# Kernel tuning notes

Measured on AMD Instinct MI355X. Metric: run time of the kernel, lower is better.

Reference implementation:

```python
import jax, jax.numpy as jnp
import numpy as np

B, CIN, H, W = 4, 1024, 64, 64
PLANES = 256
K = 3
DIL = 2
PAD = DIL * (K - 1) // 2  # = 2
EPS = 1e-5


def setup_inputs() -> dict:
    key = jax.random.key(0)
    ks = jax.random.split(key, 16)
    d = {}
    d['x'] = jax.random.normal(ks[0], (B, CIN, H, W), dtype=jnp.float32)
    # conv1: 1x1, inplanes->planes, no bias
    d['w1'] = jax.random.normal(ks[1], (PLANES, CIN), dtype=jnp.float32) * 0.02
    d['gamma1'] = jnp.ones((PLANES,), jnp.float32)
    d['beta1'] = jnp.zeros((PLANES,), jnp.float32)
    d['mean1'] = jax.random.normal(ks[2], (PLANES,), dtype=jnp.float32) * 0.1
    d['var1'] = jax.random.uniform(ks[3], (PLANES,), minval=0.5, maxval=1.5, dtype=jnp.float32)
    # deform_offset: 3x3 conv planes->18, with bias
    d['woff'] = jax.random.normal(ks[4], (18, PLANES, K, K), dtype=jnp.float32) * 0.01
    d['boff'] = jnp.zeros((18,), jnp.float32)
    # conv2 (deformable): 3x3 planes->planes, with bias
    d['w2'] = jax.random.normal(ks[5], (PLANES, PLANES, K, K), dtype=jnp.float32) * 0.02
    d['bconv2'] = jnp.zeros((PLANES,), jnp.float32)
    d['gamma2'] = jnp.ones((PLANES,), jnp.float32)
    d['beta2'] = jnp.zeros((PLANES,), jnp.float32)
    d['mean2'] = jax.random.normal(ks[6], (PLANES,), dtype=jnp.float32) * 0.1
    d['var2'] = jax.random.uniform(ks[7], (PLANES,), minval=0.5, maxval=1.5, dtype=jnp.float32)
    # conv3: 1x1 planes->planes*4, no bias
    d['w3'] = jax.random.normal(ks[8], (PLANES * 4, PLANES), dtype=jnp.float32) * 0.02
    d['gamma3'] = jnp.ones((PLANES * 4,), jnp.float32)
    d['beta3'] = jnp.zeros((PLANES * 4,), jnp.float32)
    d['mean3'] = jax.random.normal(ks[9], (PLANES * 4,), dtype=jnp.float32) * 0.1
    d['var3'] = jax.random.uniform(ks[10], (PLANES * 4,), minval=0.5, maxval=1.5, dtype=jnp.float32)
    return d


def _bn(x, gamma, beta, mean, var):
    # inference-mode BatchNorm over channel dim (NCHW)
    inv = jax.lax.rsqrt(var + EPS)
    return (x - mean[:, None, None]) * (inv * gamma)[:, None, None] + beta[:, None, None]


def _deform_conv(x, offset, w, b):
    # x: [B,C,H,W]; offset: [B,18,H,W] ordered (dy,dx) per kernel tap; w: [O,C,3,3]
    Bn, C, Hh, Ww = x.shape
    off = offset.reshape(Bn, K * K, 2, Hh, Ww)
    off_y, off_x = off[:, :, 0], off[:, :, 1]          # [B,9,H,W]
    kk = jnp.arange(K * K)
    base_y = (kk // K) * DIL - PAD                      # [9]
    base_x = (kk % K) * DIL - PAD
    ys = jnp.arange(Hh, dtype=x.dtype)
    xs = jnp.arange(Ww, dtype=x.dtype)
    py = base_y.astype(x.dtype)[None, :, None, None] + ys[None, None, :, None] + off_y
    px = base_x.astype(x.dtype)[None, :, None, None] + xs[None, None, None, :] + off_x

    def sample_one(img, py1, px1):
        # img [C,H,W]; py1/px1 [9,H,W] -> [C,9,H,W] bilinear with zero padding
        y0 = jnp.floor(py1)
        x0 = jnp.floor(px1)
        wy = py1 - y0
        wx = px1 - x0

        def gather(yc, xc):
            yi = yc.astype(jnp.int32)
            xi = xc.astype(jnp.int32)
            valid = ((yi >= 0) & (yi < Hh) & (xi >= 0) & (xi < Ww)).astype(img.dtype)
            yi = jnp.clip(yi, 0, Hh - 1)
            xi = jnp.clip(xi, 0, Ww - 1)
            return img[:, yi, xi] * valid[None]

        v00 = gather(y0, x0)
        v01 = gather(y0, x0 + 1)
        v10 = gather(y0 + 1, x0)
        v11 = gather(y0 + 1, x0 + 1)
        return (v00 * ((1 - wy) * (1 - wx))[None] + v01 * ((1 - wy) * wx)[None]
                + v10 * (wy * (1 - wx))[None] + v11 * (wy * wx)[None])

    sampled = jax.vmap(sample_one)(x, py, px)           # [B,C,9,H,W]
    out = jnp.einsum('bckhw,ock->bohw', sampled, w.reshape(w.shape[0], C, K * K))
    return out + b[None, :, None, None]


def reference(x, w1, gamma1, beta1, mean1, var1, woff, boff, w2, bconv2,
              gamma2, beta2, mean2, var2, w3, gamma3, beta3, mean3, var3):
    residual = x
    out = jnp.einsum('bchw,oc->bohw', x, w1)            # conv1 1x1
    out = jax.nn.relu(_bn(out, gamma1, beta1, mean1, var1))
    offset = jax.lax.conv_general_dilated(
        out, woff, window_strides=(1, 1), padding=((PAD, PAD), (PAD, PAD)),
        rhs_dilation=(DIL, DIL), dimension_numbers=('NCHW', 'OIHW', 'NCHW'))
    offset = offset + boff[None, :, None, None]
    out = _deform_conv(out, offset, w2, bconv2)
    out = jax.nn.relu(_bn(out, gamma2, beta2, mean2, var2))
    out = jnp.einsum('bchw,oc->bohw', out, w3)          # conv3 1x1
    out = _bn(out, gamma3, beta3, mean3, var3)
    return jax.nn.relu(out + residual)
```

## Files before the change

kernel.cpp:

```cpp
#include <hip/hip_runtime.h>

#define EPS_BN 1e-5f

typedef __bf16 bf16x8 __attribute__((ext_vector_type(8)));
typedef float f32x4 __attribute__((ext_vector_type(4)));

__device__ __forceinline__ unsigned short f2bf(float f) {
  union { float f; unsigned u; } v; v.f = f;
  unsigned r = v.u + 0x7fffu + ((v.u >> 16) & 1u);
  return (unsigned short)(r >> 16);
}
__device__ __forceinline__ float bf2f(unsigned short h) {
  union { unsigned u; float f; } v; v.u = ((unsigned)h) << 16;
  return v.f;
}

__global__ __launch_bounds__(256) void prep_all(
    const float* __restrict__ w1, const float* __restrict__ w2, const float* __restrict__ woff,
    const float* __restrict__ w3,
    const float* g1, const float* b1, const float* m1, const float* v1,
    const float* g2, const float* b2, const float* m2, const float* v2, const float* bconv2,
    const float* g3, const float* b3, const float* m3, const float* v3,
    unsigned short* __restrict__ w1b, unsigned short* __restrict__ w2r,
    uint4* __restrict__ act1Pz, unsigned short* __restrict__ wob,
    unsigned short* __restrict__ w3b, float* __restrict__ shift3,
    float* s1, float* h1, float* s2, float* h2) {
  int bid = blockIdx.x, tid = threadIdx.x;
  if (bid < 1024) {
    int i = bid * 256 + tid;
    w1b[i] = f2bf(w1[i]);
  } else if (bid < 3328) {
    int i = (bid - 1024) * 256 + tid;
    int o = i / 2304, r = i % 2304;
    int kk = r / 256, c = r % 256;
    w2r[i] = f2bf(w2[(size_t)o * 2304 + c * 9 + kk]);
  } else if (bid < 3592) {
    int i = (bid - 3328) * 256 + tid;
    int cell = i >> 5, q = i & 31;
    int b = cell / 528, r = cell - b * 528;
    int row, col;
    if (r < 136) { row = r / 68; col = r % 68; }
    else if (r < 272) { int rr = r - 136; row = 66 + rr / 68; col = rr % 68; }
    else { int rr = r - 272; row = 2 + (rr >> 2); int c4 = rr & 3; col = (c4 < 2) ? c4 : c4 + 64; }
    act1Pz[(((size_t)(b * 68) + row) * 68 + col) * 32 + q] = uint4{0, 0, 0, 0};
  } else if (bid < 3880) {
    int i = (bid - 3592) * 256 + tid;
    int o = i / 2304, r = i % 2304;
    int kk = r / 256, c = r % 256;
    wob[i] = (o < 18) ? f2bf(woff[(size_t)o * 2304 + c * 9 + kk]) : (unsigned short)0;
  } else if (bid < 4904) {
    int i = (bid - 3880) * 256 + tid;
    int o = i >> 8;
    float sc = rsqrtf(v3[o] + EPS_BN) * g3[o];
    w3b[i] = f2bf(w3[i] * sc);
  } else if (bid < 4908) {
    int c = (bid - 4904) * 256 + tid;
    float sc = rsqrtf(v3[c] + EPS_BN) * g3[c];
    shift3[c] = b3[c] - m3[c] * sc;
  } else {
    int c = tid;
    float sc1 = rsqrtf(v1[c] + EPS_BN) * g1[c];
    s1[c] = sc1; h1[c] = b1[c] - m1[c] * sc1;
    float sc2 = rsqrtf(v2[c] + EPS_BN) * g2[c];
    s2[c] = sc2; h2[c] = b2[c] + (bconv2[c] - m2[c]) * sc2;
  }
}

__global__ __launch_bounds__(256) void gemm1_x(
    const float* __restrict__ x, const unsigned short* __restrict__ Bm,
    unsigned short* __restrict__ part, int KH) {
  __shared__ __align__(16) char blob[16896];
  __shared__ __align__(16) unsigned short sA1[4096];
  __shared__ __align__(16) unsigned short sB1[4096];
  unsigned short* sA0 = (unsigned short*)blob;
  unsigned short* sB0 = (unsigned short*)(blob + 8192);
  float* tbuf = (float*)blob;
  int tid = threadIdx.x, lane = tid & 63, wv = tid >> 6;
  int z = blockIdx.z;
  int m0 = blockIdx.y * 128, n0 = blockIdx.x * 128;
  f32x4 acc[4][4] = {};
  int rowB = tid >> 2;
  int kcolBs = (((tid & 3) ^ (rowB & 3))) * 8;
  int px = tid & 127, chalf = tid >> 7;
  int s0w = (chalf * 2) ^ (px & 3), s1w = (chalf * 2 + 1) ^ (px & 3);
  int bb = m0 >> 12, p0 = m0 & 4095;
  const float* xa = x + (size_t)bb * 4194304 + (size_t)(chalf * 16) * 4096 + (p0 + px);
  int wm = wv & 1, wn = wv >> 1;
  int lane15 = lane & 15, quad = lane >> 4, l3 = lane & 3;

  float va[16];

#define G1_ISSUE_A(K0)                                                                    \
  {                                                                                       \
    const float* xp = xa + (size_t)(K0) * 4096;                                           \
    _Pragma("unroll") for (int j = 0; j < 16; ++j) va[j] = xp[(size_t)j * 4096];          \
  }

#define G1_ISSUE_B(DB, K0)                                                                \
  {                                                                                       \
    _Pragma("unroll") for (int r = 0; r < 2; ++r) {                                       \
      const unsigned short* gp = Bm + (size_t)(n0 + r * 64 + rowB) * 1024 + (K0) + kcolBs;\
      __builtin_amdgcn_global_load_lds((const __attribute__((address_space(1))) void*)gp, \
          (__attribute__((address_space(3))) void*)&(DB)[r * 2048 + wv * 512], 16, 0, 0); \
    }                                                                                     \
  }

#define G1_CVT_WRITE(DA)                                                                  \
  {                                                                                       \
    unsigned o8[8];                                                                       \
    _Pragma("unroll") for (int j = 0; j < 8; ++j)                                         \
      o8[j] = (unsigned)f2bf(va[2 * j]) | ((unsigned)f2bf(va[2 * j + 1]) << 16);          \
    *(uint4*)((DA) + px * 32 + s0w * 8) = uint4{o8[0], o8[1], o8[2], o8[3]};              \
    *(uint4*)((DA) + px * 32 + s1w * 8) = uint4{o8[4], o8[5], o8[6], o8[7]};              \
  }

#define G1_COMPUTE(DA, DB)                                                                \
  {                                                                                       \
    bf16x8 afr[4], bfr[4];                                                                \
    _Pragma("unroll") for (int mi = 0; mi < 4; ++mi)                                      \
      afr[mi] = *(const bf16x8*)&(DA)[(wm * 64 + mi * 16 + lane15) * 32 + (quad ^ l3) * 8]; \
    _Pragma("unroll") for (int ni = 0; ni < 4; ++ni)                                      \
      bfr[ni] = *(const bf16x8*)&(DB)[(wn * 64 + ni * 16 + lane15) * 32 + (quad ^ l3) * 8]; \
    _Pragma("unroll") for (int mi = 0; mi < 4; ++mi)                                      \
      _Pragma("unroll") for (int ni = 0; ni < 4; ++ni)                                    \
        acc[mi][ni] =                                                                     \
            __builtin_amdgcn_mfma_f32_16x16x32_bf16(afr[mi], bfr[ni], acc[mi][ni], 0, 0, 0); \
  }

#define G1_BODY(K0, AC, BC, AN, BN_)                                                      \
  {                                                                                       \
    G1_ISSUE_A(K0);                                                                       \
    G1_ISSUE_B(BN_, K0);                                                                  \
    asm volatile("s_waitcnt vmcnt(18)" ::: "memory");                                     \
    asm volatile("s_waitcnt lgkmcnt(0)" ::: "memory");                                    \
    __builtin_amdgcn_s_barrier();                                                         \
    G1_COMPUTE(AC, BC);                                                                   \
    asm volatile("s_waitcnt vmcnt(2)" ::: "memory");                                      \
    G1_CVT_WRITE(AN);                                                                     \
    __builtin_amdgcn_s_barrier();                                                         \
  }

  int kbase = z * KH;
  int nst = KH >> 5;
  G1_ISSUE_A(kbase);
  G1_ISSUE_B(sB0, kbase);
  asm volatile("s_waitcnt vmcnt(2)" ::: "memory");
  G1_CVT_WRITE(sA0);
  for (int t = 0; t + 2 < nst; t += 2) {
    G1_BODY(kbase + (t + 1) * 32, sA0, sB0, sA1, sB1);
    G1_BODY(kbase + (t + 2) * 32, sA1, sB1, sA0, sB0);
  }
  G1_BODY(kbase + (nst - 1) * 32, sA0, sB0, sA1, sB1);
  asm volatile("s_waitcnt vmcnt(0)" ::: "memory");
  asm volatile("s_waitcnt lgkmcnt(0)" ::: "memory");
  __builtin_amdgcn_s_barrier();
  G1_COMPUTE(sA1, sB1);
#undef G1_ISSUE_A
#undef G1_ISSUE_B
#undef G1_CVT_WRITE
#undef G1_COMPUTE
#undef G1_BODY

  unsigned short* outH = part + (size_t)z * 16384 * 256;
  int trow = tid >> 3;
  int tcol16 = (tid & 7) * 16;
  int growBase = m0 + (trow >> 4) * 64 + (trow & 15);
#pragma unroll
  for (int mi = 0; mi < 4; ++mi) {
    __syncthreads();
#pragma unroll
    for (int ni = 0; ni < 4; ++ni)
#pragma unroll
      for (int reg = 0; reg < 4; ++reg)
        tbuf[(wm * 16 + quad * 4 + reg) * 132 + wn * 64 + ni * 16 + lane15] = acc[mi][ni][reg];
    __syncthreads();
    int gr = growBase + mi * 16;
    const float* lp = &tbuf[trow * 132 + tcol16];
    unsigned o[8];
#pragma unroll
    for (int j = 0; j < 8; ++j)
      o[j] = (unsigned)f2bf(lp[2 * j]) | ((unsigned)f2bf(lp[2 * j + 1]) << 16);
    unsigned short* op = outH + (size_t)gr * 256 + n0 + tcol16;
    *(uint4*)(op) = uint4{o[0], o[1], o[2], o[3]};
    *(uint4*)(op + 8) = uint4{o[4], o[5], o[6], o[7]};
  }
}

__global__ __launch_bounds__(256) void gemm_split(
    const unsigned short* __restrict__ A, const unsigned short* __restrict__ Bm,
    unsigned short* __restrict__ part, int M, int N, int K, int KH) {
  __shared__ __align__(16) char blob[16896];
  __shared__ __align__(16) unsigned short sA1[4096];
  __shared__ __align__(16) unsigned short sB1[4096];
  __shared__ __align__(16) unsigned short sA2[4096];
  __shared__ __align__(16) unsigned short sB2[4096];
  __shared__ __align__(16) unsigned short sA3[4096];
  __shared__ __align__(16) unsigned short sB3[4096];
  unsigned short* sA0 = (unsigned short*)blob;
  unsigned short* sB0 = (unsigned short*)(blob + 8192);
  float* tbuf = (float*)blob;
  int tid = threadIdx.x, lane = tid & 63, wv = tid >> 6;
  int z = blockIdx.z;
  int m0 = blockIdx.y * 128, n0 = blockIdx.x * 128;
  f32x4 acc[4][4] = {};
  int rowA = tid >> 2;
  int kcolS = (((tid & 3) ^ (rowA & 3))) * 8;
  int wm = wv & 1, wn = wv >> 1;
  int lane15 = lane & 15, quad = lane >> 4, l3 = lane & 3;

#define GS_STAGE(dA, dB, K0)                                                              \
  {                                                                                       \
    int k0_ = (K0);                                                                       \
    _Pragma("unroll") for (int r = 0; r < 2; ++r) {                                       \
      const unsigned short* gp = A + (size_t)(m0 + r * 64 + rowA) * K + k0_ + kcolS;      \
      __builtin_amdgcn_global_load_lds((const __attribute__((address_space(1))) void*)gp, \
          (__attribute__((address_space(3))) void*)&(dA)[r * 2048 + wv * 512], 16, 0, 0); \
    }                                                                                     \
    _Pragma("unroll") for (int r = 0; r < 2; ++r) {                                       \
      const unsigned short* gp = Bm + (size_t)(n0 + r * 64 + rowA) * K + k0_ + kcolS;     \
      __builtin_amdgcn_global_load_lds((const __attribute__((address_space(1))) void*)gp, \
          (__attribute__((address_space(3))) void*)&(dB)[r * 2048 + wv * 512], 16, 0, 0); \
    }                                                                                     \
  }

#define GS_COMPUTE(dA, dB)                                                                \
  {                                                                                       \
    bf16x8 afr[4], bfr[4];                                                                \
    _Pragma("unroll") for (int mi = 0; mi < 4; ++mi)                                      \
      afr[mi] = *(const bf16x8*)&(dA)[(wm * 64 + mi * 16 + lane15) * 32 + (quad ^ l3) * 8]; \
    _Pragma("unroll") for (int ni = 0; ni < 4; ++ni)                                      \
      bfr[ni] = *(const bf16x8*)&(dB)[(wn * 64 + ni * 16 + lane15) * 32 + (quad ^ l3) * 8]; \
    _Pragma("unroll") for (int mi = 0; mi < 4; ++mi)                                      \
      _Pragma("unroll") for (int ni = 0; ni < 4; ++ni)                                    \
        acc[mi][ni] =                                                                     \
            __builtin_amdgcn_mfma_f32_16x16x32_bf16(afr[mi], bfr[ni], acc[mi][ni], 0, 0, 0); \
  }

#define GS_STEP8(AC, BC, SN, AN, BN_)                                                     \
  {                                                                                       \
    GS_STAGE(AN, BN_, kbase + (SN) * 32);                                                 \
    asm volatile("s_waitcnt vmcnt(8)" ::: "memory");                                      \
    __builtin_amdgcn_s_barrier();                                                         \
    GS_COMPUTE(AC, BC);                                                                   \
    __builtin_amdgcn_s_barrier();                                                         \
  }

  int kbase = z * KH;
  int nst = KH >> 5;
  GS_STAGE(sA0, sB0, kbase);
  GS_STAGE(sA1, sB1, kbase + 32);
  for (int s4 = 0; s4 < nst - 4; s4 += 4) {
    GS_STEP8(sA0, sB0, s4 + 2, sA2, sB2);
    GS_STEP8(sA1, sB1, s4 + 3, sA3, sB3);
    GS_STEP8(sA2, sB2, s4 + 4, sA0, sB0);
    GS_STEP8(sA3, sB3, s4 + 5, sA1, sB1);
  }
  GS_STEP8(sA0, sB0, nst - 2, sA2, sB2);
  GS_STEP8(sA1, sB1, nst - 1, sA3, sB3);
  asm volatile("s_waitcnt vmcnt(4)" ::: "memory");
  __builtin_amdgcn_s_barrier();
  GS_COMPUTE(sA2, sB2);
  __builtin_amdgcn_s_barrier();
  asm volatile("s_waitcnt vmcnt(0)" ::: "memory");
  __builtin_amdgcn_s_barrier();
  GS_COMPUTE(sA3, sB3);
  __builtin_amdgcn_s_barrier();
#undef GS_STAGE
#undef GS_COMPUTE
#undef GS_STEP8

  unsigned short* outH = part + (size_t)z * M * N;
  int trow = tid >> 3;
  int tcol16 = (tid & 7) * 16;
  int growBase = m0 + (trow >> 4) * 64 + (trow & 15);
#pragma unroll
  for (int mi = 0; mi < 4; ++mi) {
    __syncthreads();
#pragma unroll
    for (int ni = 0; ni < 4; ++ni)
#pragma unroll
      for (int reg = 0; reg < 4; ++reg)
        tbuf[(wm * 16 + quad * 4 + reg) * 132 + wn * 64 + ni * 16 + lane15] = acc[mi][ni][reg];
    __syncthreads();
    int gr = growBase + mi * 16;
    const float* lp = &tbuf[trow * 132 + tcol16];
    unsigned o[8];
#pragma unroll
    for (int j = 0; j < 8; ++j)
      o[j] = (unsigned)f2bf(lp[2 * j]) | ((unsigned)f2bf(lp[2 * j + 1]) << 16);
    unsigned short* op = outH + (size_t)gr * 256 + n0 + tcol16;
    *(uint4*)(op) = uint4{o[0], o[1], o[2], o[3]};
    *(uint4*)(op + 8) = uint4{o[4], o[5], o[6], o[7]};
  }
}

template <int NS, int PAD>
__global__ __launch_bounds__(256) void epi_bn(const unsigned short* __restrict__ part,
                                              const float* __restrict__ scale,
                                              const float* __restrict__ shift,
                                              unsigned short* __restrict__ outT,
                                              unsigned short* __restrict__ outP) {
  int gid = blockIdx.x * 256 + threadIdx.x;
  int row = gid >> 5, c0 = (gid & 31) * 8;
  float v[8] = {};
#pragma unroll
  for (int s = 0; s < NS; ++s) {
    uint4 q = *(const uint4*)(part + (size_t)s * 16384 * 256 + (size_t)row * 256 + c0);
    unsigned u[4] = {q.x, q.y, q.z, q.w};
#pragma unroll
    for (int j = 0; j < 4; ++j) {
      v[2 * j]     += bf2f((unsigned short)(u[j] & 0xffffu));
      v[2 * j + 1] += bf2f((unsigned short)(u[j] >> 16));
    }
  }
  float sc[8], sh[8];
  *(float4*)&sc[0] = *(const float4*)(scale + c0); *(float4*)&sc[4] = *(const float4*)(scale + c0 + 4);
  *(float4*)&sh[0] = *(const float4*)(shift + c0); *(float4*)&sh[4] = *(const float4*)(shift + c0 + 4);
  unsigned o[4];
#pragma unroll
  for (int j = 0; j < 4; ++j) {
    float lo = fmaxf(v[2 * j] * sc[2 * j] + sh[2 * j], 0.f);
    float hi = fmaxf(v[2 * j + 1] * sc[2 * j + 1] + sh[2 * j + 1], 0.f);
    o[j] = (unsigned)f2bf(lo) | ((unsigned)f2bf(hi) << 16);
  }
  uint4 pk{o[0], o[1], o[2], o[3]};
  *(uint4*)(outT + (size_t)row * 256 + c0) = pk;
  if constexpr (PAD) {
    int bb = row >> 12, p = row & 4095;
    *(uint4*)(outP + (((size_t)(bb * 68) + (p >> 6) + 2) * 68 + (p & 63) + 2) * 256 + c0) = pk;
  }
}

__global__ __launch_bounds__(256) void gemm_res(
    const unsigned short* __restrict__ A, const unsigned short* __restrict__ Bm,
    float* __restrict__ outp, const float* __restrict__ shift3,
    const float* __restrict__ resid, int M, int N, int K, long bStrideB, long bStrideOut) {
  __shared__ __align__(16) char blob[16896];
  __shared__ __align__(16) unsigned short sA1[4096];
  __shared__ __align__(16) unsigned short sB1[4096];
  unsigned short* sA0 = (unsigned short*)blob;
  unsigned short* sB0 = (unsigned short*)(blob + 8192);
  float* tbuf = (float*)blob;
  int tid = threadIdx.x, lane = tid & 63, wv = tid >> 6;
  int z = blockIdx.z;
  const unsigned short* Bz = Bm + (size_t)z * bStrideB;
  int m0 = blockIdx.y * 128, n0 = blockIdx.x * 128;
  f32x4 acc[4][4] = {};
  int rowA = tid >> 2;
  int kcolS = (((tid & 3) ^ (rowA & 3))) * 8;
  int wm = wv & 1, wn = wv >> 1;
  int lane15 = lane & 15, quad = lane >> 4, l3 = lane & 3;

#define GR_STAGE(dA, dB, K0)                                                              \
  {                                                                                       \
    int k0_ = (K0);                                                                       \
    _Pragma("unroll") for (int r = 0; r < 2; ++r) {                                       \
      const unsigned short* gp = A + (size_t)(m0 + r * 64 + rowA) * K + k0_ + kcolS;      \
      __builtin_amdgcn_global_load_lds((const __attribute__((address_space(1))) void*)gp, \
          (__attribute__((address_space(3))) void*)&(dA)[r * 2048 + wv * 512], 16, 0, 0); \
    }                                                                                     \
    _Pragma("unroll") for (int r = 0; r < 2; ++r) {                                       \
      const unsigned short* gp = Bz + (size_t)(n0 + r * 64 + rowA) * K + k0_ + kcolS;     \
      __builtin_amdgcn_global_load_lds((const __attribute__((address_space(1))) void*)gp, \
          (__attribute__((address_space(3))) void*)&(dB)[r * 2048 + wv * 512], 16, 0, 0); \
    }                                                                                     \
  }

#define GR_COMPUTE(dA, dB)                                                                \
  {                                                                                       \
    bf16x8 afr[4], bfr[4];                                                                \
    _Pragma("unroll") for (int mi = 0; mi < 4; ++mi)                                      \
      afr[mi] = *(const bf16x8*)&(dA)[(wm * 64 + mi * 16 + lane15) * 32 + (quad ^ l3) * 8]; \
    _Pragma("unroll") for (int ni = 0; ni < 4; ++ni)                                      \
      bfr[ni] = *(const bf16x8*)&(dB)[(wn * 64 + ni * 16 + lane15) * 32 + (quad ^ l3) * 8]; \
    _Pragma("unroll") for (int mi = 0; mi < 4; ++mi)                                      \
      _Pragma("unroll") for (int ni = 0; ni < 4; ++ni)                                    \
        acc[mi][ni] =                                                                     \
            __builtin_amdgcn_mfma_f32_16x16x32_bf16(afr[mi], bfr[ni], acc[mi][ni], 0, 0, 0); \
  }

  int nst = K >> 5;
  GR_STAGE(sA0, sB0, 0);
  for (int t = 0; t < nst; t += 2) {
    GR_STAGE(sA1, sB1, (t + 1) * 32);
    asm volatile("s_waitcnt vmcnt(4)" ::: "memory");
    __builtin_amdgcn_s_barrier();
    GR_COMPUTE(sA0, sB0);
    __builtin_amdgcn_s_barrier();
    if (t + 2 < nst) {
      GR_STAGE(sA0, sB0, (t + 2) * 32);
      asm volatile("s_waitcnt vmcnt(4)" ::: "memory");
    } else {
      asm volatile("s_waitcnt vmcnt(0)" ::: "memory");
    }
    __builtin_amdgcn_s_barrier();
    GR_COMPUTE(sA1, sB1);
    __builtin_amdgcn_s_barrier();
  }
#undef GR_STAGE
#undef GR_COMPUTE

  float* outF = outp + (size_t)z * bStrideOut;
  const float* res = resid + (size_t)z * bStrideOut;
  int trow = tid >> 3;
  int tcol = (tid & 7) * 4;
  int growBase = m0 + (trow >> 4) * 64 + (trow & 15);
#pragma unroll
  for (int mi = 0; mi < 4; ++mi) {
    __syncthreads();
#pragma unroll
    for (int ni = 0; ni < 4; ++ni)
#pragma unroll
      for (int reg = 0; reg < 4; ++reg)
        tbuf[(wm * 16 + quad * 4 + reg) * 132 + wn * 64 + ni * 16 + lane15] = acc[mi][ni][reg];
    __syncthreads();
    int gr = growBase + mi * 16;
    float sh = shift3[gr];
    const float* rp = res + (size_t)gr * N + n0 + tcol;
    float* op = outF + (size_t)gr * N + n0 + tcol;
    const float* lp = &tbuf[trow * 132 + tcol];
#pragma unroll
    for (int j = 0; j < 4; ++j) {
      float4 rv = *(const float4*)(rp + j * 32);
      float4 lv = *(const float4*)(lp + j * 32);
      float4 ov;
      ov.x = fmaxf(lv.x + sh + rv.x, 0.f);
      ov.y = fmaxf(lv.y + sh + rv.y, 0.f);
      ov.z = fmaxf(lv.z + sh + rv.z, 0.f);
      ov.w = fmaxf(lv.w + sh + rv.w, 0.f);
      *(float4*)(op + j * 32) = ov;
    }
  }
}

__global__ __launch_bounds__(256) void off_gemm(const unsigned short* __restrict__ actP,
                                                const unsigned short* __restrict__ wob,
                                                const float* __restrict__ boff,
                                                float* __restrict__ offsP) {
  __shared__ __align__(16) unsigned short sA0[4096];
  __shared__ __align__(16) unsigned short sA1[4096];
  __shared__ __align__(16) unsigned short sA2[4096];
  __shared__ __align__(16) unsigned short sA3[4096];
  __shared__ __align__(16) unsigned short sB0[2048];
  __shared__ __align__(16) unsigned short sB1[2048];
  __shared__ __align__(16) unsigned short sB2[2048];
  __shared__ __align__(16) unsigned short sB3[2048];
  int tid = threadIdx.x, lane = tid & 63, wv = tid >> 6;
  int m0 = blockIdx.x * 64;
  int lane15 = lane & 15, quad8 = (lane >> 4) * 8;
  int rowA = tid >> 3;
  int kc = (tid & 7) * 8;

  const unsigned short* baseA[2];
#pragma unroll
  for (int r = 0; r < 2; ++r) {
    int row = m0 + r * 32 + rowA;
    int b = row >> 12, p = row & 4095;
    baseA[r] = actP + (((size_t)(b * 68) + (p >> 6) + 2) * 68 + (p & 63) + 2) * 256 + kc;
  }
  const unsigned short* baseB = wob + (size_t)rowA * 2304 + kc;

  f32x4 acc[2] = {};

#define OG_STAGE(dA, dB, S)                                                               \
  {                                                                                       \
    int s_ = (S); int kk_ = s_ >> 2; int c0_ = (s_ & 3) * 64;                             \
    long shift_ = (long)(((kk_ / 3) * 2 - 2) * 68 + ((kk_ % 3) * 2 - 2));                 \
    _Pragma("unroll") for (int r = 0; r < 2; ++r) {                                       \
      const unsigned short* gp = baseA[r] + shift_ * 256 + c0_;                           \
      __builtin_amdgcn_global_load_lds((const __attribute__((address_space(1))) void*)gp, \
          (__attribute__((address_space(3))) void*)&(dA)[r * 2048 + wv * 512], 16, 0, 0); \
    }                                                                                     \
    {                                                                                     \
      const unsigned short* gp = baseB + kk_ * 256 + c0_;                                 \
      __builtin_amdgcn_global_load_lds((const __attribute__((address_space(1))) void*)gp, \
          (__attribute__((address_space(3))) void*)&(dB)[wv * 512], 16, 0, 0);            \
    }                                                                                     \
  }

#define OG_COMPUTE(dA, dB)                                                                \
  {                                                                                       \
    bf16x8 afr[2], bfr[2][2];                                                             \
    _Pragma("unroll") for (int kq = 0; kq < 2; ++kq) {                                    \
      afr[kq] = *(const bf16x8*)&(dA)[(wv * 16 + lane15) * 64 + kq * 32 + quad8];         \
      _Pragma("unroll") for (int ni = 0; ni < 2; ++ni)                                    \
        bfr[kq][ni] = *(const bf16x8*)&(dB)[(ni * 16 + lane15) * 64 + kq * 32 + quad8];   \
    }                                                                                     \
    _Pragma("unroll") for (int kq = 0; kq < 2; ++kq)                                      \
      _Pragma("unroll") for (int ni = 0; ni < 2; ++ni)                                    \
        acc[ni] = __builtin_amdgcn_mfma_f32_16x16x32_bf16(afr[kq], bfr[kq][ni], acc[ni], 0, 0, 0); \
  }

#define OG_STEP6(AC, BC, SN, AN, BN_)                                                     \
  {                                                                                       \
    OG_STAGE(AN, BN_, SN);                                                                \
    asm volatile("s_waitcnt vmcnt(6)" ::: "memory");                                      \
    __builtin_amdgcn_s_barrier();                                                         \
    OG_COMPUTE(AC, BC);                                                                   \
    __builtin_amdgcn_s_barrier();                                                        \
  }

  OG_STAGE(sA0, sB0, 0);
  OG_STAGE(sA1, sB1, 1);
  for (int s4 = 0; s4 < 32; s4 += 4) {
    OG_STEP6(sA0, sB0, s4 + 2, sA2, sB2);
    OG_STEP6(sA1, sB1, s4 + 3, sA3, sB3);
    OG_STEP6(sA2, sB2, s4 + 4, sA0, sB0);
    OG_STEP6(sA3, sB3, s4 + 5, sA1, sB1);
  }
  OG_STEP6(sA0, sB0, 34, sA2, sB2);
  OG_STEP6(sA1, sB1, 35, sA3, sB3);
  asm volatile("s_waitcnt vmcnt(3)" ::: "memory");
  __builtin_amdgcn_s_barrier();
  OG_COMPUTE(sA2, sB2);
  __builtin_amdgcn_s_barrier();
  asm volatile("s_waitcnt vmcnt(0)" ::: "memory");
  __builtin_amdgcn_s_barrier();
  OG_COMPUTE(sA3, sB3);
#undef OG_STAGE
#undef OG_COMPUTE
#undef OG_STEP6

#pragma unroll
  for (int ni = 0; ni < 2; ++ni) {
    int o = ni * 16 + lane15;
    if (o < 18) {
      float bo = boff[o];
#pragma unroll
      for (int reg = 0; reg < 4; ++reg) {
        int row = m0 + wv * 16 + (lane >> 4) * 4 + reg;
        offsP[(size_t)row * 18 + o] = acc[ni][reg] + bo;
      }
    }
  }
}

__global__ __launch_bounds__(256) void deform_sample(const unsigned short* __restrict__ act1T,
                                                     const float* __restrict__ offsP,
                                                     unsigned short* __restrict__ S) {
  int g = threadIdx.x >> 5, t = threadIdx.x & 31;
  int idx = blockIdx.x * 8 + g;
  int b = idx >> 12, p = idx & 4095;
  int h = p >> 6, w = p & 63;
  const unsigned short* actb = act1T + (size_t)b * 4096 * 256 + t * 8;
  unsigned short* Sp = S + (size_t)idx * 2304 + t * 8;
  float ov = (t < 18) ? offsP[(size_t)idx * 18 + t] : 0.f;
#pragma unroll
  for (int kk = 0; kk < 9; ++kk) {
    float offy = __shfl(ov, 2 * kk, 32);
    float offx = __shfl(ov, 2 * kk + 1, 32);
    float py = (float)(h + (kk / 3) * 2 - 2) + offy;
    float px = (float)(w + (kk % 3) * 2 - 2) + offx;
    float fy = floorf(py), fx = floorf(px);
    int y0 = (int)fy, x0 = (int)fx;
    float wy = py - fy, wx = px - fx;
    bool yv0 = (y0 >= 0 && y0 < 64), yv1 = (y0 >= -1 && y0 < 63);
    bool xv0 = (x0 >= 0 && x0 < 64), xv1 = (x0 >= -1 && x0 < 63);
    const unsigned short* cb = actb + (y0 * 64 + x0) * 256;
    uint4 q00{0,0,0,0}, q01{0,0,0,0}, q10{0,0,0,0}, q11{0,0,0,0};
    if (yv0 && xv0) q00 = *(const uint4*)(cb);
    if (yv0 && xv1) q01 = *(const uint4*)(cb + 256);
    if (yv1 && xv0) q10 = *(const uint4*)(cb + 64 * 256);
    if (yv1 && xv1) q11 = *(const uint4*)(cb + 64 * 256 + 256);
    float w00 = (1.f - wy) * (1.f - wx), w01 = (1.f - wy) * wx;
    float w10 = wy * (1.f - wx), w11 = wy * wx;
    unsigned u00[4] = {q00.x, q00.y, q00.z, q00.w};
    unsigned u01[4] = {q01.x, q01.y, q01.z, q01.w};
    unsigned u10[4] = {q10.x, q10.y, q10.z, q10.w};
    unsigned u11[4] = {q11.x, q11.y, q11.z, q11.w};
    unsigned out[4];
#pragma unroll
    for (int j = 0; j < 4; ++j) {
      float lo = bf2f((unsigned short)(u00[j] & 0xffffu)) * w00 +
                 bf2f((unsigned short)(u01[j] & 0xffffu)) * w01 +
                 bf2f((unsigned short)(u10[j] & 0xffffu)) * w10 +
                 bf2f((unsigned short)(u11[j] & 0xffffu)) * w11;
      float hi = bf2f((unsigned short)(u00[j] >> 16)) * w00 +
                 bf2f((unsigned short)(u01[j] >> 16)) * w01 +
                 bf2f((unsigned short)(u10[j] >> 16)) * w10 +
                 bf2f((unsigned short)(u11[j] >> 16)) * w11;
      out[j] = (unsigned)f2bf(lo) | ((unsigned)f2bf(hi) << 16);
    }
    *(uint4*)(Sp + kk * 256) = uint4{out[0], out[1], out[2], out[3]};
  }
}

extern "C" void kernel_launch(void* const* d_in, const int* in_sizes, int n_in,
                              void* d_out, int out_size, void* d_ws, size_t ws_size,
                              hipStream_t stream) {
  const float* x      = (const float*)d_in[0];
  const float* w1     = (const float*)d_in[1];
  const float* gamma1 = (const float*)d_in[2];
  const float* beta1  = (const float*)d_in[3];
  const float* mean1  = (const float*)d_in[4];
  const float* var1   = (const float*)d_in[5];
  const float* woff   = (const float*)d_in[6];
  const float* boff   = (const float*)d_in[7];
  const float* w2     = (const float*)d_in[8];
  const float* bconv2 = (const float*)d_in[9];
  const float* gamma2 = (const float*)d_in[10];
  const float* beta2  = (const float*)d_in[11];
  const float* mean2  = (const float*)d_in[12];
  const float* var2   = (const float*)d_in[13];
  const float* w3     = (const float*)d_in[14];
  const float* gamma3 = (const float*)d_in[15];
  const float* beta3  = (const float*)d_in[16];
  const float* mean3  = (const float*)d_in[17];
  const float* var3   = (const float*)d_in[18];

  char* ws = (char*)d_ws;
  unsigned short* act1T = (unsigned short*)(ws + 33554432);
  unsigned short* act2T = (unsigned short*)(ws + 41943040);
  unsigned short* S     = (unsigned short*)(ws + 50331648);
  float*          offs  = (float*)(ws + 125829120);
  unsigned short* w1b   = (unsigned short*)(ws + 127008768);
  unsigned short* w2r   = (unsigned short*)(ws + 127533056);
  unsigned short* w3b   = (unsigned short*)(ws + 128712704);
  float*          bnS1  = (float*)(ws + 129236992);
  float*          bnH1  = (float*)(ws + 129238016);
  float*          bnS2  = (float*)(ws + 129239040);
  float*          bnH2  = (float*)(ws + 129240064);
  float*          shift3= (float*)(ws + 129241088);
  unsigned short* act1P = S;
  unsigned short* part1 = (unsigned short*)(ws + 62914560);
  unsigned short* part2 = (unsigned short*)ws;
  unsigned short* wob   = act2T;

  prep_all<<<4909, 256, 0, stream>>>(w1, w2, woff, w3,
                                     gamma1, beta1, mean1, var1,
                                     gamma2, beta2, mean2, var2, bconv2,
                                     gamma3, beta3, mean3, var3,
                                     w1b, w2r, (uint4*)act1P, wob, w3b, shift3,
                                     bnS1, bnH1, bnS2, bnH2);

  gemm1_x<<<dim3(2, 128, 2), 256, 0, stream>>>(x, w1b, part1, 512);
  epi_bn<2, 1><<<2048, 256, 0, stream>>>(part1, bnS1, bnH1, act1T, act1P);

  off_gemm<<<256, 256, 0, stream>>>(act1P, wob, boff, offs);
  deform_sample<<<dim3(2048), 256, 0, stream>>>(act1T, offs, S);

  gemm_split<<<dim3(2, 128, 2), 256, 0, stream>>>(S, w2r, part2, 16384, 256, 2304, 1152);
  epi_bn<2, 0><<<2048, 256, 0, stream>>>(part2, bnS2, bnH2, act2T, nullptr);

  gemm_res<<<dim3(32, 8, 4), 256, 0, stream>>>(w3b, act2T, (float*)d_out, shift3, x,
                                               1024, 4096, 256, 4096L * 256, 4194304L);
}
```

Measured before the change: 270.3 us.

## Drop split-K in conv1 and deform GEMMs, fuse BN+ReLU epilogue into GEMMs

The two GEMMs (conv1 and the deformable conv) no longer split K across two blocks. Each block now runs the full K range and applies BN scale/shift plus ReLU directly in its epilogue, and the separate epi_bn reduction kernels are removed. This saves the bf16 partial-sum writes and reads and two kernel launches. It also removes the rounding of partials to bf16 before summation. The cost is half as many blocks per GEMM (256), so there is less parallelism on a large-CU GPU. gemm1 gains a deeper double-buffered register/LDS pipeline with extra B buffers to compensate.

Measured after the change: 272.5 us. No clear change (+0.8%).

```diff
diff --git a/kernel.cpp b/kernel.cpp
--- a/kernel.cpp
+++ b/kernel.cpp
@@ -66,17 +66,19 @@
   }
 }
 
-__global__ __launch_bounds__(256) void gemm1_x(
+__global__ __launch_bounds__(256) void gemm1f(
     const float* __restrict__ x, const unsigned short* __restrict__ Bm,
-    unsigned short* __restrict__ part, int KH) {
+    const float* __restrict__ scale, const float* __restrict__ shift,
+    unsigned short* __restrict__ outT, unsigned short* __restrict__ outP) {
   __shared__ __align__(16) char blob[16896];
   __shared__ __align__(16) unsigned short sA1[4096];
   __shared__ __align__(16) unsigned short sB1[4096];
+  __shared__ __align__(16) unsigned short sB2[4096];
+  __shared__ __align__(16) unsigned short sB3[4096];
   unsigned short* sA0 = (unsigned short*)blob;
   unsigned short* sB0 = (unsigned short*)(blob + 8192);
   float* tbuf = (float*)blob;
   int tid = threadIdx.x, lane = tid & 63, wv = tid >> 6;
-  int z = blockIdx.z;
   int m0 = blockIdx.y * 128, n0 = blockIdx.x * 128;
   f32x4 acc[4][4] = {};
   int rowB = tid >> 2;
@@ -88,12 +90,12 @@
   int wm = wv & 1, wn = wv >> 1;
   int lane15 = lane & 15, quad = lane >> 4, l3 = lane & 3;
 
-  float va[16];
-
-#define G1_ISSUE_A(K0)                                                                    \
+  float va0[16], va1[16];
+
+#define G1_ISSUE_A(VA, K0)                                                                \
   {                                                                                       \
     const float* xp = xa + (size_t)(K0) * 4096;                                           \
-    _Pragma("unroll") for (int j = 0; j < 16; ++j) va[j] = xp[(size_t)j * 4096];          \
+    _Pragma("unroll") for (int j = 0; j < 16; ++j) (VA)[j] = xp[(size_t)j * 4096];        \
   }
 
 #define G1_ISSUE_B(DB, K0)                                                                \
@@ -105,11 +107,11 @@
     }                                                                                     \
   }
 
-#define G1_CVT_WRITE(DA)                                                                  \
+#define G1_CVT_WRITE(VA, DA)                                                              \
   {                                                                                       \
     unsigned o8[8];                                                                       \
     _Pragma("unroll") for (int j = 0; j < 8; ++j)                                         \
-      o8[j] = (unsigned)f2bf(va[2 * j]) | ((unsigned)f2bf(va[2 * j + 1]) << 16);          \
+      o8[j] = (unsigned)f2bf((VA)[2 * j]) | ((unsigned)f2bf((VA)[2 * j + 1]) << 16);      \
     *(uint4*)((DA) + px * 32 + s0w * 8) = uint4{o8[0], o8[1], o8[2], o8[3]};              \
     *(uint4*)((DA) + px * 32 + s1w * 8) = uint4{o8[4], o8[5], o8[6], o8[7]};              \
   }
@@ -127,43 +129,57 @@
             __builtin_amdgcn_mfma_f32_16x16x32_bf16(afr[mi], bfr[ni], acc[mi][ni], 0, 0, 0); \
   }
 
-#define G1_BODY(K0, AC, BC, AN, BN_)                                                      \
-  {                                                                                       \
-    G1_ISSUE_A(K0);                                                                       \
-    G1_ISSUE_B(BN_, K0);                                                                  \
-    asm volatile("s_waitcnt vmcnt(18)" ::: "memory");                                     \
+#define G1F_BODY(VAI, VAC, AC, AW, BC, BI, K2)                                            \
+  {                                                                                       \
+    G1_ISSUE_A(VAI, K2);                                                                  \
+    G1_ISSUE_B(BI, K2);                                                                   \
+    asm volatile("s_waitcnt vmcnt(20)" ::: "memory");                                     \
     asm volatile("s_waitcnt lgkmcnt(0)" ::: "memory");                                    \
     __builtin_amdgcn_s_barrier();                                                         \
     G1_COMPUTE(AC, BC);                                                                   \
-    asm volatile("s_waitcnt vmcnt(2)" ::: "memory");                                      \
-    G1_CVT_WRITE(AN);                                                                     \
+    G1_CVT_WRITE(VAC, AW);                                                                \
     __builtin_amdgcn_s_barrier();                                                         \
   }
 
-  int kbase = z * KH;
-  int nst = KH >> 5;
-  G1_ISSUE_A(kbase);
-  G1_ISSUE_B(sB0, kbase);
+  G1_ISSUE_A(va0, 0);
+  G1_ISSUE_B(sB0, 0);
   asm volatile("s_waitcnt vmcnt(2)" ::: "memory");
-  G1_CVT_WRITE(sA0);
-  for (int t = 0; t + 2 < nst; t += 2) {
-    G1_BODY(kbase + (t + 1) * 32, sA0, sB0, sA1, sB1);
-    G1_BODY(kbase + (t + 2) * 32, sA1, sB1, sA0, sB0);
-  }
-  G1_BODY(kbase + (nst - 1) * 32, sA0, sB0, sA1, sB1);
+  G1_CVT_WRITE(va0, sA0);
+  G1_ISSUE_A(va1, 32);
+  G1_ISSUE_B(sB1, 32);
+  for (int t = 0; t < 28; t += 4) {
+    G1F_BODY(va0, va1, sA0, sA1, sB0, sB2, (t + 2) * 32);
+    G1F_BODY(va1, va0, sA1, sA0, sB1, sB3, (t + 3) * 32);
+    G1F_BODY(va0, va1, sA0, sA1, sB2, sB0, (t + 4) * 32);
+    G1F_BODY(va1, va0, sA1, sA0, sB3, sB1, (t + 5) * 32);
+  }
+  G1F_BODY(va0, va1, sA0, sA1, sB0, sB2, 30 * 32);
+  G1F_BODY(va1, va0, sA1, sA0, sB1, sB3, 31 * 32);
+  asm volatile("s_waitcnt vmcnt(2)" ::: "memory");
+  asm volatile("s_waitcnt lgkmcnt(0)" ::: "memory");
+  __builtin_amdgcn_s_barrier();
+  G1_COMPUTE(sA0, sB2);
+  G1_CVT_WRITE(va1, sA1);
+  __builtin_amdgcn_s_barrier();
   asm volatile("s_waitcnt vmcnt(0)" ::: "memory");
   asm volatile("s_waitcnt lgkmcnt(0)" ::: "memory");
   __builtin_amdgcn_s_barrier();
-  G1_COMPUTE(sA1, sB1);
+  G1_COMPUTE(sA1, sB3);
 #undef G1_ISSUE_A
 #undef G1_ISSUE_B
 #undef G1_CVT_WRITE
 #undef G1_COMPUTE
-#undef G1_BODY
-
-  unsigned short* outH = part + (size_t)z * 16384 * 256;
+#undef G1F_BODY
+
   int trow = tid >> 3;
   int tcol16 = (tid & 7) * 16;
+  int c0e = n0 + tcol16;
+  float sc[16], sh[16];
+#pragma unroll
+  for (int q = 0; q < 4; ++q) {
+    *(float4*)&sc[q * 4] = *(const float4*)(scale + c0e + q * 4);
+    *(float4*)&sh[q * 4] = *(const float4*)(shift + c0e + q * 4);
+  }
   int growBase = m0 + (trow >> 4) * 64 + (trow & 15);
 #pragma unroll
   for (int mi = 0; mi < 4; ++mi) {
@@ -178,17 +194,26 @@
     const float* lp = &tbuf[trow * 132 + tcol16];
     unsigned o[8];
 #pragma unroll
-    for (int j = 0; j < 8; ++j)
-      o[j] = (unsigned)f2bf(lp[2 * j]) | ((unsigned)f2bf(lp[2 * j + 1]) << 16);
-    unsigned short* op = outH + (size_t)gr * 256 + n0 + tcol16;
-    *(uint4*)(op) = uint4{o[0], o[1], o[2], o[3]};
-    *(uint4*)(op + 8) = uint4{o[4], o[5], o[6], o[7]};
-  }
-}
-
-__global__ __launch_bounds__(256) void gemm_split(
+    for (int j = 0; j < 8; ++j) {
+      float lo = fmaxf(lp[2 * j] * sc[2 * j] + sh[2 * j], 0.f);
+      float hi = fmaxf(lp[2 * j + 1] * sc[2 * j + 1] + sh[2 * j + 1], 0.f);
+      o[j] = (unsigned)f2bf(lo) | ((unsigned)f2bf(hi) << 16);
+    }
+    uint4 pk0{o[0], o[1], o[2], o[3]}, pk1{o[4], o[5], o[6], o[7]};
+    unsigned short* op = outT + (size_t)gr * 256 + c0e;
+    *(uint4*)(op) = pk0;
+    *(uint4*)(op + 8) = pk1;
+    int b2 = gr >> 12, p = gr & 4095;
+    unsigned short* pp = outP + (((size_t)(b2 * 68) + (p >> 6) + 2) * 68 + (p & 63) + 2) * 256 + c0e;
+    *(uint4*)(pp) = pk0;
+    *(uint4*)(pp + 8) = pk1;
+  }
+}
+
+__global__ __launch_bounds__(256) void gemm2f(
     const unsigned short* __restrict__ A, const unsigned short* __restrict__ Bm,
-    unsigned short* __restrict__ part, int M, int N, int K, int KH) {
+    const float* __restrict__ scale, const float* __restrict__ shift,
+    unsigned short* __restrict__ outT) {
   __shared__ __align__(16) char blob[16896];
   __shared__ __align__(16) unsigned short sA1[4096];
   __shared__ __align__(16) unsigned short sB1[4096];
@@ -200,7 +225,6 @@
   unsigned short* sB0 = (unsigned short*)(blob + 8192);
   float* tbuf = (float*)blob;
   int tid = threadIdx.x, lane = tid & 63, wv = tid >> 6;
-  int z = blockIdx.z;
   int m0 = blockIdx.y * 128, n0 = blockIdx.x * 128;
   f32x4 acc[4][4] = {};
   int rowA = tid >> 2;
@@ -212,12 +236,12 @@
   {                                                                                       \
     int k0_ = (K0);                                                                       \
     _Pragma("unroll") for (int r = 0; r < 2; ++r) {                                       \
-      const unsigned short* gp = A + (size_t)(m0 + r * 64 + rowA) * K + k0_ + kcolS;      \
+      const unsigned short* gp = A + (size_t)(m0 + r * 64 + rowA) * 2304 + k0_ + kcolS;   \
       __builtin_amdgcn_global_load_lds((const __attribute__((address_space(1))) void*)gp, \
           (__attribute__((address_space(3))) void*)&(dA)[r * 2048 + wv * 512], 16, 0, 0); \
     }                                                                                     \
     _Pragma("unroll") for (int r = 0; r < 2; ++r) {                                       \
-      const unsigned short* gp = Bm + (size_t)(n0 + r * 64 + rowA) * K + k0_ + kcolS;     \
+      const unsigned short* gp = Bm + (size_t)(n0 + r * 64 + rowA) * 2304 + k0_ + kcolS;  \
       __builtin_amdgcn_global_load_lds((const __attribute__((address_space(1))) void*)gp, \
           (__attribute__((address_space(3))) void*)&(dB)[r * 2048 + wv * 512], 16, 0, 0); \
     }                                                                                     \
@@ -238,17 +262,16 @@
 
 #define GS_STEP8(AC, BC, SN, AN, BN_)                                                     \
   {                                                                                       \
-    GS_STAGE(AN, BN_, kbase + (SN) * 32);                                                 \
+    GS_STAGE(AN, BN_, (SN) * 32);                                                         \
     asm volatile("s_waitcnt vmcnt(8)" ::: "memory");                                      \
     __builtin_amdgcn_s_barrier();                                                         \
     GS_COMPUTE(AC, BC);                                                                   \
     __builtin_amdgcn_s_barrier();                                                         \
   }
 
-  int kbase = z * KH;
-  int nst = KH >> 5;
-  GS_STAGE(sA0, sB0, kbase);
-  GS_STAGE(sA1, sB1, kbase + 32);
+  const int nst = 72;
+  GS_STAGE(sA0, sB0, 0);
+  GS_STAGE(sA1, sB1, 32);
   for (int s4 = 0; s4 < nst - 4; s4 += 4) {
     GS_STEP8(sA0, sB0, s4 + 2, sA2, sB2);
     GS_STEP8(sA1, sB1, s4 + 3, sA3, sB3);
@@ -269,9 +292,15 @@
 #undef GS_COMPUTE
 #undef GS_STEP8
 
-  unsigned short* outH = part + (size_t)z * M * N;
   int trow = tid >> 3;
   int tcol16 = (tid & 7) * 16;
+  int c0e = n0 + tcol16;
+  float sc[16], sh[16];
+#pragma unroll
+  for (int q = 0; q < 4; ++q) {
+    *(float4*)&sc[q * 4] = *(const float4*)(scale + c0e + q * 4);
+    *(float4*)&sh[q * 4] = *(const float4*)(shift + c0e + q * 4);
+  }
   int growBase = m0 + (trow >> 4) * 64 + (trow & 15);
 #pragma unroll
   for (int mi = 0; mi < 4; ++mi) {
@@ -286,48 +315,14 @@
     const float* lp = &tbuf[trow * 132 + tcol16];
     unsigned o[8];
 #pragma unroll
-    for (int j = 0; j < 8; ++j)
-      o[j] = (unsigned)f2bf(lp[2 * j]) | ((unsigned)f2bf(lp[2 * j + 1]) << 16);
-    unsigned short* op = outH + (size_t)gr * 256 + n0 + tcol16;
+    for (int j = 0; j < 8; ++j) {
+      float lo = fmaxf(lp[2 * j] * sc[2 * j] + sh[2 * j], 0.f);
+      float hi = fmaxf(lp[2 * j + 1] * sc[2 * j + 1] + sh[2 * j + 1], 0.f);
+      o[j] = (unsigned)f2bf(lo) | ((unsigned)f2bf(hi) << 16);
+    }
+    unsigned short* op = outT + (size_t)gr * 256 + c0e;
     *(uint4*)(op) = uint4{o[0], o[1], o[2], o[3]};
     *(uint4*)(op + 8) = uint4{o[4], o[5], o[6], o[7]};
-  }
-}
-
-template <int NS, int PAD>
-__global__ __launch_bounds__(256) void epi_bn(const unsigned short* __restrict__ part,
-                                              const float* __restrict__ scale,
-                                              const float* __restrict__ shift,
-                                              unsigned short* __restrict__ outT,
-                                              unsigned short* __restrict__ outP) {
-  int gid = blockIdx.x * 256 + threadIdx.x;
-  int row = gid >> 5, c0 = (gid & 31) * 8;
-  float v[8] = {};
-#pragma unroll
-  for (int s = 0; s < NS; ++s) {
-    uint4 q = *(const uint4*)(part + (size_t)s * 16384 * 256 + (size_t)row * 256 + c0);
-    unsigned u[4] = {q.x, q.y, q.z, q.w};
-#pragma unroll
-    for (int j = 0; j < 4; ++j) {
-      v[2 * j]     += bf2f((unsigned short)(u[j] & 0xffffu));
-      v[2 * j + 1] += bf2f((unsigned short)(u[j] >> 16));
-    }
-  }
-  float sc[8], sh[8];
-  *(float4*)&sc[0] = *(const float4*)(scale + c0); *(float4*)&sc[4] = *(const float4*)(scale + c0 + 4);
-  *(float4*)&sh[0] = *(const float4*)(shift + c0); *(float4*)&sh[4] = *(const float4*)(shift + c0 + 4);
-  unsigned o[4];
-#pragma unroll
-  for (int j = 0; j < 4; ++j) {
-    float lo = fmaxf(v[2 * j] * sc[2 * j] + sh[2 * j], 0.f);
-    float hi = fmaxf(v[2 * j + 1] * sc[2 * j + 1] + sh[2 * j + 1], 0.f);
-    o[j] = (unsigned)f2bf(lo) | ((unsigned)f2bf(hi) << 16);
-  }
-  uint4 pk{o[0], o[1], o[2], o[3]};
-  *(uint4*)(outT + (size_t)row * 256 + c0) = pk;
-  if constexpr (PAD) {
-    int bb = row >> 12, p = row & 4095;
-    *(uint4*)(outP + (((size_t)(bb * 68) + (p >> 6) + 2) * 68 + (p & 63) + 2) * 256 + c0) = pk;
   }
 }
 
@@ -497,7 +492,7 @@
     asm volatile("s_waitcnt vmcnt(6)" ::: "memory");                                      \
     __builtin_amdgcn_s_barrier();                                                         \
     OG_COMPUTE(AC, BC);                                                                   \
-    __builtin_amdgcn_s_barrier();                                                        \
+    __builtin_amdgcn_s_barrier();                                                         \
   }
 
   OG_STAGE(sA0, sB0, 0);
@@ -622,8 +617,6 @@
   float*          bnH2  = (float*)(ws + 129240064);
   float*          shift3= (float*)(ws + 129241088);
   unsigned short* act1P = S;
-  unsigned short* part1 = (unsigned short*)(ws + 62914560);
-  unsigned short* part2 = (unsigned short*)ws;
   unsigned short* wob   = act2T;
 
   prep_all<<<4909, 256, 0, stream>>>(w1, w2, woff, w3,
@@ -633,14 +626,12 @@
                                      w1b, w2r, (uint4*)act1P, wob, w3b, shift3,
                                      bnS1, bnH1, bnS2, bnH2);
 
-  gemm1_x<<<dim3(2, 128, 2), 256, 0, stream>>>(x, w1b, part1, 512);
-  epi_bn<2, 1><<<2048, 256, 0, stream>>>(part1, bnS1, bnH1, act1T, act1P);
+  gemm1f<<<dim3(2, 128), 256, 0, stream>>>(x, w1b, bnS1, bnH1, act1T, act1P);
 
   off_gemm<<<256, 256, 0, stream>>>(act1P, wob, boff, offs);
   deform_sample<<<dim3(2048), 256, 0, stream>>>(act1T, offs, S);
 
-  gemm_split<<<dim3(2, 128, 2), 256, 0, stream>>>(S, w2r, part2, 16384, 256, 2304, 1152);
-  epi_bn<2, 0><<<2048, 256, 0, stream>>>(part2, bnS2, bnH2, act2T, nullptr);
+  gemm2f<<<dim3(2, 128), 256, 0, stream>>>(S, w2r, bnS2, bnH2, act2T);
 
   gemm_res<<<dim3(32, 8, 4), 256, 0, stream>>>(w3b, act2T, (float*)d_out, shift3, x,
                                                1024, 4096, 256, 4096L * 256, 4194304L);
```
